# Optimization experiments

Measured on AMD Instinct MI355X. Metric: run time of the kernel, lower is better.

The kernel has to match this reference:

```python
import jax, jax.numpy as jnp
import numpy as np
import math

B, S, D, H = 2, 2048, 2048, 16
HD = D // H  # head_dim = 128


def _rope_tables(seq_len, head_dim, theta=10000.0):
    inv = 1.0 / (theta ** (np.arange(0, head_dim, 2, dtype=np.float32) / head_dim))
    t = np.arange(seq_len, dtype=np.float32)
    freqs = np.outer(t, inv)  # [S, HD/2]
    return jnp.asarray(np.cos(freqs)), jnp.asarray(np.sin(freqs))


def setup_inputs() -> dict:
    key = jax.random.key(0)
    ks = jax.random.split(key, 6)
    std = 1.0 / math.sqrt(D)
    x = jax.random.normal(ks[0], (B, S, D), dtype=jnp.float32)
    wq_w = jax.random.normal(ks[1], (D, D), dtype=jnp.float32) * std
    wk_w = jax.random.normal(ks[2], (D, D), dtype=jnp.float32) * std
    wv_w = jax.random.normal(ks[3], (D, D), dtype=jnp.float32) * std
    wo_w = jax.random.normal(ks[4], (D, D), dtype=jnp.float32) * std
    zb = jnp.zeros((D,), dtype=jnp.float32)
    fc, fs = _rope_tables(S, HD)
    return {"x": x, "wq_w": wq_w, "wq_b": zb, "wk_w": wk_w, "wk_b": zb,
            "wv_w": wv_w, "wv_b": zb, "wo_w": wo_w, "wo_b": zb,
            "freqs_cos": fc, "freqs_sin": fs}


def _apply_rope(q, k, cos, sin):
    # q, k: [B, S, H, HD]; cos/sin: [S, HD/2] -> broadcast [1, S, 1, HD/2]
    cos = cos[None, :, None, :]
    sin = sin[None, :, None, :]

    def rot(t):
        tr, ti = t[..., 0::2], t[..., 1::2]
        orr = tr * cos - ti * sin
        oi = tr * sin + ti * cos
        return jnp.stack([orr, oi], axis=-1).reshape(t.shape)

    return rot(q), rot(k)


def reference(x, wq_w, wq_b, wk_w, wk_b, wv_w, wv_b, wo_w, wo_b, freqs_cos, freqs_sin):
    b, s, d = x.shape
    q = (x @ wq_w.T + wq_b).reshape(b, s, H, HD)
    k = (x @ wk_w.T + wk_b).reshape(b, s, H, HD)
    v = (x @ wv_w.T + wv_b).reshape(b, s, H, HD)
    q, k = _apply_rope(q, k, freqs_cos[:s], freqs_sin[:s])
    q = q.transpose(0, 2, 1, 3)  # [B,H,S,HD]
    k = k.transpose(0, 2, 1, 3)
    v = v.transpose(0, 2, 1, 3)
    scale = math.sqrt(HD)
    scores = jnp.einsum('bhqd,bhkd->bhqk', q, k) / scale
    causal = jnp.tril(jnp.ones((s, s), dtype=bool))
    scores = jnp.where(causal[None, None], scores, jnp.float32(-jnp.inf))
    attn = jax.nn.softmax(scores, axis=-1)
    out = jnp.einsum('bhqk,bhkd->bhqd', attn, v)
    out = out.transpose(0, 2, 1, 3).reshape(b, s, d)
    out = out @ wo_w.T + wo_b
    return out, k, v
```

## Files before the change

### kernel.cpp

```cpp
#include <hip/hip_runtime.h>

#define B_  2
#define S_  2048
#define D_  2048
#define H_  16
#define HD_ 128

#define QSCALE 0.1275174319003887f

typedef __attribute__((ext_vector_type(4))) float  f32x4;
typedef __attribute__((ext_vector_type(8))) short  short8;
typedef __attribute__((ext_vector_type(8))) __bf16 bf16x8;
typedef __attribute__((ext_vector_type(4))) float  floatv4;
typedef __attribute__((ext_vector_type(4))) unsigned short ushortv4;

__device__ inline unsigned short f2bf(float f) {
  unsigned int u = __builtin_bit_cast(unsigned int, f);
  u += 0x7fffu + ((u >> 16) & 1u);
  return (unsigned short)(u >> 16);
}

__device__ inline void gld16(void* lds, const void* g) {
  __builtin_amdgcn_global_load_lds(
      (const __attribute__((address_space(1))) unsigned int*)g,
      (__attribute__((address_space(3))) unsigned int*)lds, 16, 0, 0);
}

__device__ inline bf16x8 lds_frag_b(const void* p) {
  return __builtin_bit_cast(bf16x8, *(const short8*)p);
}

__global__ void cvt_all(const float* __restrict__ x,
                        const float* __restrict__ w0, const float* __restrict__ w1,
                        const float* __restrict__ w2, const float* __restrict__ w3,
                        unsigned short* __restrict__ xb,
                        unsigned short* __restrict__ wb0, unsigned short* __restrict__ wb1,
                        unsigned short* __restrict__ wb2, unsigned short* __restrict__ wb3) {
  int i = blockIdx.x * 256 + threadIdx.x;
  const float* s; unsigned short* d; int off;
  if (i < 2097152) { s = x; d = xb; off = i; }
  else {
    int j = i - 2097152;
    int r = j >> 20; off = j & 1048575;
    s = (r == 0) ? w0 : (r == 1) ? w1 : (r == 2) ? w2 : w3;
    d = (r == 0) ? wb0 : (r == 1) ? wb1 : (r == 2) ? wb2 : wb3;
  }
  floatv4 v = ((const floatv4*)s)[off];
  ushortv4 o;
  o.x = f2bf(v.x); o.y = f2bf(v.y); o.z = f2bf(v.z); o.w = f2bf(v.w);
  ((ushortv4*)d)[off] = o;
}

template<int MI0, int NJ0>
__device__ inline void quad_mm(f32x4 (&acc)[4][4], const bf16x8 (&af)[2][2], const bf16x8 (&bf)[2][2]) {
#pragma unroll
  for (int mi = 0; mi < 2; ++mi)
#pragma unroll
    for (int nj = 0; nj < 2; ++nj)
#pragma unroll
      for (int ks = 0; ks < 2; ++ks)
        acc[MI0 + mi][NJ0 + nj] =
            __builtin_amdgcn_mfma_f32_16x16x32_bf16(af[mi][ks], bf[nj][ks], acc[MI0 + mi][NJ0 + nj], 0, 0, 0);
}

__device__ inline void stage(char* ldsbuf, int chunk, const char* gtile, int w, long thrOff) {
  gld16(ldsbuf + chunk * 8192 + w * 1024, gtile + (long)chunk * 64 * 4096 + thrOff);
}

#define RDF(dst, buf, baserow)                                                          \
  do {                                                                                  \
    int _r0 = (baserow);                                                                \
    _Pragma("unroll") for (int _ii = 0; _ii < 2; ++_ii) {                               \
      int _row = _r0 + _ii * 16;                                                        \
      _Pragma("unroll") for (int _ks = 0; _ks < 2; ++_ks)                               \
          dst[_ii][_ks] = lds_frag_b((buf) + _row * 128 + ((_ks * 64 + quad * 16) ^ xsw)); \
    }                                                                                   \
  } while (0)

#define GBAR() __builtin_amdgcn_s_barrier()
#define LGK0()                                                 \
  do {                                                         \
    asm volatile("s_waitcnt lgkmcnt(0)" ::: "memory");         \
    __builtin_amdgcn_sched_barrier(0);                         \
  } while (0)

template<int MODE>
__global__ __launch_bounds__(512, 1)
void gemm8p(const unsigned short* __restrict__ A,
            const unsigned short* __restrict__ W,
            const float* __restrict__ b0, const float* __restrict__ b1, const float* __restrict__ b2,
            float* __restrict__ CQ,
            float* __restrict__ CK,
            float* __restrict__ v_out,
            int nbx) {
  __shared__ __attribute__((aligned(16))) char smem[98304];
  char* As0 = smem;
  char* As1 = smem + 32768;
  char* Bs0 = smem + 65536;
  char* Bs1 = smem + 81920;

  const int t = threadIdx.x, w = t >> 6, lane = t & 63;
  const int quad = lane >> 4, l16 = lane & 15;
  const int wm = (w >> 1) * 64, wn = (w & 1) * 64;
  const int xsw = (l16 & 7) << 4;

  const int nwg = gridDim.x, q8 = nwg >> 3;
  const int wg = ((int)blockIdx.x & 7) * q8 + ((int)blockIdx.x >> 3);
  const int by = wg / nbx, bx = wg % nbx;
  const int m0 = by * 256, n0 = bx * 128;

  const char* Agl = (const char*)A + (size_t)m0 * 4096;
  const char* Wgl = (const char*)W + (size_t)n0 * 4096;
  const int sr = t >> 3;
  const long thrOff = (long)sr * 4096 + (((t & 7) * 16) ^ ((sr & 7) << 4));

#pragma unroll
  for (int c = 0; c < 4; ++c) stage(As0, c, Agl, w, thrOff);
#pragma unroll
  for (int c = 0; c < 2; ++c) stage(Bs0, c, Wgl, w, thrOff);
#pragma unroll
  for (int c = 0; c < 4; ++c) stage(As1, c, Agl + 128, w, thrOff);
  asm volatile("s_waitcnt vmcnt(4)" ::: "memory");
  GBAR();

  f32x4 acc[4][4] = {};

  for (int it = 0; it < 16; ++it) {
    int s0p = 2 * it + 2; if (s0p >= 32) s0p -= 2;
    int s1p = 2 * it + 3; if (s1p >= 32) s1p -= 2;
    const char* gB1  = Wgl + (long)(2 * it + 1) * 128;
    const char* gA0p = Agl + (long)s0p * 128;
    const char* gB0p = Wgl + (long)s0p * 128;
    const char* gA1p = Agl + (long)s1p * 128;
    bf16x8 a01[2][2], a23[2][2], b01[2][2], b23[2][2];

    stage(Bs1, 0, gB1, w, thrOff); stage(Bs1, 1, gB1, w, thrOff);
    RDF(a01, As0, wm + l16);
    RDF(a23, As0, wm + 32 + l16);
    RDF(b01, Bs0, wn + l16);
    GBAR(); LGK0();
    __builtin_amdgcn_s_setprio(1);
    quad_mm<0, 0>(acc, a01, b01); quad_mm<2, 0>(acc, a23, b01);
    __builtin_amdgcn_s_setprio(0);
    GBAR();
    RDF(b23, Bs0, wn + 32 + l16);
    stage(As0, 0, gA0p, w, thrOff); stage(As0, 1, gA0p, w, thrOff);
    stage(As0, 2, gA0p, w, thrOff); stage(As0, 3, gA0p, w, thrOff);
    GBAR(); LGK0();
    __builtin_amdgcn_s_setprio(1);
    quad_mm<0, 2>(acc, a01, b23); quad_mm<2, 2>(acc, a23, b23);
    __builtin_amdgcn_s_setprio(0);
    asm volatile("s_waitcnt vmcnt(4)" ::: "memory");
    GBAR();
    RDF(a01, As1, wm + l16);
    RDF(a23, As1, wm + 32 + l16);
    RDF(b01, Bs1, wn + l16);
    stage(Bs0, 0, gB0p, w, thrOff); stage(Bs0, 1, gB0p, w, thrOff);
    GBAR(); LGK0();
    __builtin_amdgcn_s_setprio(1);
    quad_mm<0, 0>(acc, a01, b01); quad_mm<2, 0>(acc, a23, b01);
    __builtin_amdgcn_s_setprio(0);
    GBAR();
    RDF(b23, Bs1, wn + 32 + l16);
    stage(As1, 0, gA1p, w, thrOff); stage(As1, 1, gA1p, w, thrOff);
    stage(As1, 2, gA1p, w, thrOff); stage(As1, 3, gA1p, w, thrOff);
    GBAR(); LGK0();
    __builtin_amdgcn_s_setprio(1);
    quad_mm<0, 2>(acc, a01, b23); quad_mm<2, 2>(acc, a23, b23);
    __builtin_amdgcn_s_setprio(0);
    asm volatile("s_waitcnt vmcnt(4)" ::: "memory");
    GBAR();
  }

  asm volatile("s_waitcnt vmcnt(0)" ::: "memory");

  if constexpr (MODE == 1) {
#pragma unroll
    for (int nj = 0; nj < 4; ++nj) {
      int col = n0 + wn + nj * 16 + l16;
      int sel = col >> 11;
      int cc  = col & 2047;
      const float* bp = (sel == 0) ? b0 : (sel == 1) ? b1 : b2;
      float bv = bp[cc];
#pragma unroll
      for (int mi = 0; mi < 4; ++mi)
#pragma unroll
        for (int r = 0; r < 4; ++r) {
          int row = m0 + wm + mi * 16 + quad * 4 + r;
          float v = acc[mi][nj][r] + bv;
          if (sel == 0) {
            CQ[(size_t)row * 2048 + cc] = v;
          } else if (sel == 1) {
            CK[(size_t)row * 2048 + cc] = v;
          } else {
            int s = row & 2047, bb = row >> 11;
            int hh = cc >> 7, d = cc & 127;
            v_out[((size_t)(bb * H_ + hh) * S_ + s) * HD_ + d] = v;
          }
        }
    }
  } else {
#pragma unroll
    for (int nj = 0; nj < 4; ++nj) {
      int col = n0 + wn + nj * 16 + l16;
      float bv = b0[col];
#pragma unroll
      for (int mi = 0; mi < 4; ++mi)
#pragma unroll
        for (int r = 0; r < 4; ++r) {
          int row = m0 + wm + mi * 16 + quad * 4 + r;
          CQ[(size_t)row * 2048 + col] = acc[mi][nj][r] + bv;
        }
    }
  }
}

__global__ void rope_kernel(const float* __restrict__ Qbuf,
                            const float* __restrict__ Kbuf,
                            const float* __restrict__ fc,
                            const float* __restrict__ fs,
                            unsigned short* __restrict__ Qa,
                            unsigned short* __restrict__ Ka,
                            float* __restrict__ k_out) {
  int idx = blockIdx.x * 256 + threadIdx.x;
  int i = idx & 63;
  int h = (idx >> 6) & (H_ - 1);
  int s = (idx >> 10) & (S_ - 1);
  int b = idx >> 21;
  size_t src = ((size_t)(b * S_ + s)) * D_ + h * HD_ + 2 * i;
  float2 q = *(const float2*)(Qbuf + src);
  float2 k = *(const float2*)(Kbuf + src);
  float c = fc[s * 64 + i], sn = fs[s * 64 + i];
  float qor = q.x * c - q.y * sn, qoi = q.x * sn + q.y * c;
  float kor = k.x * c - k.y * sn, koi = k.x * sn + k.y * c;
  size_t dst = ((size_t)((b * H_ + h) * S_ + s)) * HD_ + 2 * i;
  *(unsigned int*)(Qa + dst) = (unsigned int)f2bf(qor * QSCALE) | ((unsigned int)f2bf(qoi * QSCALE) << 16);
  *(unsigned int*)(Ka + dst) = (unsigned int)f2bf(kor) | ((unsigned int)f2bf(koi) << 16);
  *(float2*)(k_out + dst) = make_float2(kor, koi);
}

__global__ void vtrans_kernel(const float* __restrict__ Vsrc,
                              unsigned short* __restrict__ Vt) {
  __shared__ float tile[64][33];
  int t = threadIdx.x;
  int s0 = blockIdx.x * 64, d0 = blockIdx.y * 32, bh = blockIdx.z;
#pragma unroll
  for (int rr = 0; rr < 8; ++rr) {
    int sl = rr * 8 + (t >> 5), dl = t & 31;
    tile[sl][dl] = Vsrc[((size_t)(bh * S_ + s0 + sl)) * HD_ + d0 + dl];
  }
  __syncthreads();
#pragma unroll
  for (int rr = 0; rr < 8; ++rr) {
    int dl = rr * 4 + (t >> 6), sl = t & 63;
    Vt[((size_t)(bh * HD_ + d0 + dl)) * S_ + s0 + sl] = f2bf(tile[sl][dl]);
  }
}

__global__ __launch_bounds__(256, 2)
void attn_kernel(const unsigned short* __restrict__ Qa,
                 const unsigned short* __restrict__ Ka,
                 const unsigned short* __restrict__ Vt,
                 unsigned short* __restrict__ Oa) {
  __shared__ __attribute__((aligned(16))) unsigned short Ks[2][64 * 128];
  __shared__ __attribute__((aligned(16))) unsigned short Vs[128 * 64];
  __shared__ __attribute__((aligned(16))) unsigned short Ps[4][16 * 64];
  const int t = threadIdx.x, w = t >> 6, lane = t & 63;
  const int quad = lane >> 4, l16 = lane & 15;
  const int bid = blockIdx.x;
  const int bh = (bid & 7) + 8 * (bid >> 7);
  const int p  = (bid >> 3) & 15;
  const int b = bh >> 4, h = bh & 15;
  const unsigned short* Qp = Qa + (size_t)bh * S_ * HD_;
  const unsigned short* Kp = Ka + (size_t)bh * S_ * HD_;
  const unsigned short* Vp = Vt + (size_t)bh * HD_ * S_;
  const float NEGINF = -__builtin_inff();

  for (int part = 0; part < 2; ++part) {
    const int qs = part ? (31 - p) : p;
    const int q0 = qs * 64;
    const int ntmax = qs;

    __syncthreads();

#pragma unroll
    for (int j = 0; j < 4; ++j) {
      int o = (t + 256 * j) * 16;
      int row = o >> 8, cb = (o & 255) ^ ((row & 7) << 4);
      gld16((char*)Ks[0] + w * 1024 + j * 4096, (const char*)(Kp + (size_t)row * HD_) + cb);
    }
    bf16x8 qf[4];
#pragma unroll
    for (int kk = 0; kk < 4; ++kk)
      qf[kk] = *(const bf16x8*)(Qp + (size_t)(q0 + w * 16 + l16) * HD_ + kk * 32 + quad * 8);

    float m_i[4], l_i[4];
#pragma unroll
    for (int r = 0; r < 4; ++r) { m_i[r] = NEGINF; l_i[r] = 0.f; }
    f32x4 oacc[8] = {};
    int c = 0;

    for (int nt = 0; nt <= ntmax; ++nt) {
      __syncthreads();

#pragma unroll
      for (int j = 0; j < 4; ++j) {
        int o = (t + 256 * j) * 16;
        int vrow = o >> 7, vcb = (o & 127) ^ ((vrow & 7) << 4);
        gld16((char*)Vs + w * 1024 + j * 4096,
              (const char*)(Vp + (size_t)vrow * S_ + nt * 64) + vcb);
      }

      f32x4 sacc[4] = {};
      const char* Kc = (const char*)Ks[c];
#pragma unroll
      for (int j = 0; j < 4; ++j) {
        int krow = j * 16 + l16;
        const char* kbase = Kc + krow * 256;
        int ksw = (krow & 7) << 4;
#pragma unroll
        for (int kk = 0; kk < 4; ++kk) {
          bf16x8 kf = lds_frag_b(kbase + ((kk * 64 + quad * 16) ^ ksw));
          sacc[j] = __builtin_amdgcn_mfma_f32_16x16x32_bf16(qf[kk], kf, sacc[j], 0, 0, 0);
        }
      }

      const bool dotail = (nt == ntmax);
      float rowmax[4], alpha[4], rowsum[4];
#pragma unroll
      for (int r = 0; r < 4; ++r) rowmax[r] = NEGINF;
#pragma unroll
      for (int j = 0; j < 4; ++j) {
        int scol = nt * 64 + j * 16 + l16;
#pragma unroll
        for (int r = 0; r < 4; ++r) {
          float v = sacc[j][r];
          if (dotail && scol > q0 + w * 16 + quad * 4 + r) v = NEGINF;
          sacc[j][r] = v;
          rowmax[r] = fmaxf(rowmax[r], v);
        }
      }
#pragma unroll
      for (int off = 1; off < 16; off <<= 1)
#pragma unroll
        for (int r = 0; r < 4; ++r)
          rowmax[r] = fmaxf(rowmax[r], __shfl_xor(rowmax[r], off));
#pragma unroll
      for (int r = 0; r < 4; ++r) {
        float mnew = fmaxf(m_i[r], rowmax[r]);
        alpha[r] = __builtin_amdgcn_exp2f(m_i[r] - mnew);
        m_i[r] = mnew;
        rowsum[r] = 0.f;
      }
#pragma unroll
      for (int j = 0; j < 4; ++j)
#pragma unroll
        for (int r = 0; r < 4; ++r) {
          float e = __builtin_amdgcn_exp2f(sacc[j][r] - m_i[r]);
          sacc[j][r] = e;
          rowsum[r] += e;
        }
#pragma unroll
      for (int off = 1; off < 16; off <<= 1)
#pragma unroll
        for (int r = 0; r < 4; ++r)
          rowsum[r] += __shfl_xor(rowsum[r], off);
#pragma unroll
      for (int r = 0; r < 4; ++r) l_i[r] = l_i[r] * alpha[r] + rowsum[r];
#pragma unroll
      for (int f = 0; f < 8; ++f)
#pragma unroll
        for (int r = 0; r < 4; ++r) oacc[f][r] *= alpha[r];

      __syncthreads();

      if (nt < ntmax) {
#pragma unroll
        for (int j = 0; j < 4; ++j) {
          int o = (t + 256 * j) * 16;
          int row = o >> 8, cb = (o & 255) ^ ((row & 7) << 4);
          gld16((char*)Ks[c ^ 1] + w * 1024 + j * 4096,
                (const char*)(Kp + (size_t)((nt + 1) * 64 + row) * HD_) + cb);
        }
      }

      char* Pw = (char*)&Ps[w][0];
#pragma unroll
      for (int j = 0; j < 4; ++j)
#pragma unroll
        for (int r = 0; r < 4; ++r) {
          int prow = quad * 4 + r;
          *(unsigned short*)(Pw + prow * 128 + ((2 * (j * 16 + l16)) ^ ((prow & 7) << 4))) = f2bf(sacc[j][r]);
        }
      asm volatile("s_waitcnt lgkmcnt(0)" ::: "memory");

      const char* Vb = (const char*)Vs;
      int psw = (l16 & 7) << 4;
#pragma unroll
      for (int s2 = 0; s2 < 2; ++s2) {
        bf16x8 pf = lds_frag_b(Pw + l16 * 128 + ((s2 * 64 + quad * 16) ^ psw));
#pragma unroll
        for (int f = 0; f < 8; ++f) {
          int vrow = f * 16 + l16;
          bf16x8 vf = lds_frag_b(Vb + vrow * 128 + ((s2 * 64 + quad * 16) ^ ((vrow & 7) << 4)));
          oacc[f] = __builtin_amdgcn_mfma_f32_16x16x32_bf16(pf, vf, oacc[f], 0, 0, 0);
        }
      }
      c ^= 1;
    }

    float invl[4];
#pragma unroll
    for (int r = 0; r < 4; ++r) invl[r] = 1.f / l_i[r];
#pragma unroll
    for (int f = 0; f < 8; ++f)
#pragma unroll
      for (int r = 0; r < 4; ++r) {
        int srow = q0 + w * 16 + quad * 4 + r;
        int d = f * 16 + l16;
        Oa[((size_t)(b * S_ + srow)) * D_ + h * HD_ + d] = f2bf(oacc[f][r] * invl[r]);
      }
  }
}

extern "C" void kernel_launch(void* const* d_in, const int* in_sizes, int n_in,
                              void* d_out, int out_size, void* d_ws, size_t ws_size,
                              hipStream_t stream) {
  const float* x    = (const float*)d_in[0];
  const float* wq_w = (const float*)d_in[1];
  const float* wq_b = (const float*)d_in[2];
  const float* wk_w = (const float*)d_in[3];
  const float* wk_b = (const float*)d_in[4];
  const float* wv_w = (const float*)d_in[5];
  const float* wv_b = (const float*)d_in[6];
  const float* wo_w = (const float*)d_in[7];
  const float* wo_b = (const float*)d_in[8];
  const float* fc   = (const float*)d_in[9];
  const float* fs   = (const float*)d_in[10];

  float* out = (float*)d_out;
  const size_t BSD = (size_t)B_ * S_ * D_;
  float* k_out = out + BSD;
  float* v_out = out + 2 * BSD;

  char* ws = (char*)d_ws;
  unsigned short* xb   = (unsigned short*)(ws);
  unsigned short* wqb  = (unsigned short*)(ws + 16777216);
  unsigned short* wkb  = (unsigned short*)(ws + 25165824);
  unsigned short* wvb  = (unsigned short*)(ws + 33554432);
  unsigned short* wob  = (unsigned short*)(ws + 41943040);
  float*          Kbuf = (float*)(ws + 50331648);
  unsigned short* Qat  = (unsigned short*)(ws + 83886080);
  unsigned short* Kat  = (unsigned short*)(ws + 100663296);
  unsigned short* Vt   = (unsigned short*)(ws + 117440512);
  unsigned short* Ab   = (unsigned short*)(ws + 134217728);

  float* Qbuf = out;

  cvt_all<<<24576, 256, 0, stream>>>(x, wq_w, wk_w, wv_w, wo_w, xb, wqb, wkb, wvb, wob);

  gemm8p<1><<<dim3(768), 512, 0, stream>>>(xb, wqb, wq_b, wk_b, wv_b,
                                           Qbuf, Kbuf, v_out, 48);

  rope_kernel<<<16384, 256, 0, stream>>>(Qbuf, Kbuf, fc, fs, Qat, Kat, k_out);
  vtrans_kernel<<<dim3(32, 4, 32), 256, 0, stream>>>(v_out, Vt);
  attn_kernel<<<512, 256, 0, stream>>>(Qat, Kat, Vt, Ab);

  gemm8p<0><<<dim3(256), 512, 0, stream>>>(Ab, wob, wo_b, nullptr, nullptr,
                                           out, nullptr, nullptr, 16);
}
```

Before: 438.9 us.

## Interleave GEMM MFMA phases with finer staging and skip softmax rescale when max unchanged

The projection GEMM main loop is restructured so each quad_mm is a separate barrier-delimited phase, with LDS fragment reads and global-to-LDS staging spread across those phases. The B tile for the next step is also prefetched one stage earlier, so the vmcnt waits become 6. The aim is better overlap of memory traffic with MFMA work. In the attention kernel, the online-softmax rescale of l and oacc is skipped when no row maximum in the wave grows, which saves exp and multiply work on most tiles. The cost is a divergent branch and more barriers per GEMM iteration.

New measurement: 462.3 us. +5.3%, slower.

```diff
diff --git a/kernel.cpp b/kernel.cpp
--- a/kernel.cpp
+++ b/kernel.cpp
@@ -120,55 +120,61 @@
   for (int c = 0; c < 2; ++c) stage(Bs0, c, Wgl, w, thrOff);
 #pragma unroll
   for (int c = 0; c < 4; ++c) stage(As1, c, Agl + 128, w, thrOff);
-  asm volatile("s_waitcnt vmcnt(4)" ::: "memory");
+#pragma unroll
+  for (int c = 0; c < 2; ++c) stage(Bs1, c, Wgl + 128, w, thrOff);
+  asm volatile("s_waitcnt vmcnt(6)" ::: "memory");
   GBAR();
 
   f32x4 acc[4][4] = {};
 
   for (int it = 0; it < 16; ++it) {
-    int s0p = 2 * it + 2; if (s0p >= 32) s0p -= 2;
-    int s1p = 2 * it + 3; if (s1p >= 32) s1p -= 2;
-    const char* gB1  = Wgl + (long)(2 * it + 1) * 128;
-    const char* gA0p = Agl + (long)s0p * 128;
-    const char* gB0p = Wgl + (long)s0p * 128;
-    const char* gA1p = Agl + (long)s1p * 128;
+    int s0 = 2 * it + 2; if (s0 >= 32) s0 -= 2;
+    int s1 = 2 * it + 3; if (s1 >= 32) s1 -= 2;
+    const char* As0g = Agl + (long)s0 * 128;
+    const char* Bs0g = Wgl + (long)s0 * 128;
+    const char* As1g = Agl + (long)s1 * 128;
+    const char* Bs1g = Wgl + (long)s1 * 128;
     bf16x8 a01[2][2], a23[2][2], b01[2][2], b23[2][2];
 
-    stage(Bs1, 0, gB1, w, thrOff); stage(Bs1, 1, gB1, w, thrOff);
     RDF(a01, As0, wm + l16);
+    RDF(b01, Bs0, wn + l16);
+    GBAR(); LGK0();
+    __builtin_amdgcn_s_setprio(1); quad_mm<0, 0>(acc, a01, b01); __builtin_amdgcn_s_setprio(0);
+    GBAR();
     RDF(a23, As0, wm + 32 + l16);
-    RDF(b01, Bs0, wn + l16);
-    GBAR(); LGK0();
-    __builtin_amdgcn_s_setprio(1);
-    quad_mm<0, 0>(acc, a01, b01); quad_mm<2, 0>(acc, a23, b01);
-    __builtin_amdgcn_s_setprio(0);
+    GBAR(); LGK0();
+    __builtin_amdgcn_s_setprio(1); quad_mm<2, 0>(acc, a23, b01); __builtin_amdgcn_s_setprio(0);
     GBAR();
     RDF(b23, Bs0, wn + 32 + l16);
-    stage(As0, 0, gA0p, w, thrOff); stage(As0, 1, gA0p, w, thrOff);
-    stage(As0, 2, gA0p, w, thrOff); stage(As0, 3, gA0p, w, thrOff);
-    GBAR(); LGK0();
-    __builtin_amdgcn_s_setprio(1);
-    quad_mm<0, 2>(acc, a01, b23); quad_mm<2, 2>(acc, a23, b23);
-    __builtin_amdgcn_s_setprio(0);
+    stage(As0, 0, As0g, w, thrOff); stage(As0, 1, As0g, w, thrOff);
+    GBAR(); LGK0();
+    __builtin_amdgcn_s_setprio(1); quad_mm<0, 2>(acc, a01, b23); __builtin_amdgcn_s_setprio(0);
+    GBAR();
+    stage(As0, 2, As0g, w, thrOff); stage(As0, 3, As0g, w, thrOff);
+    GBAR(); LGK0();
+    __builtin_amdgcn_s_setprio(1); quad_mm<2, 2>(acc, a23, b23); __builtin_amdgcn_s_setprio(0);
     asm volatile("s_waitcnt vmcnt(4)" ::: "memory");
     GBAR();
     RDF(a01, As1, wm + l16);
+    RDF(b01, Bs1, wn + l16);
+    stage(Bs0, 0, Bs0g, w, thrOff); stage(Bs0, 1, Bs0g, w, thrOff);
+    GBAR(); LGK0();
+    __builtin_amdgcn_s_setprio(1); quad_mm<0, 0>(acc, a01, b01); __builtin_amdgcn_s_setprio(0);
+    GBAR();
     RDF(a23, As1, wm + 32 + l16);
-    RDF(b01, Bs1, wn + l16);
-    stage(Bs0, 0, gB0p, w, thrOff); stage(Bs0, 1, gB0p, w, thrOff);
-    GBAR(); LGK0();
-    __builtin_amdgcn_s_setprio(1);
-    quad_mm<0, 0>(acc, a01, b01); quad_mm<2, 0>(acc, a23, b01);
-    __builtin_amdgcn_s_setprio(0);
+    GBAR(); LGK0();
+    __builtin_amdgcn_s_setprio(1); quad_mm<2, 0>(acc, a23, b01); __builtin_amdgcn_s_setprio(0);
     GBAR();
     RDF(b23, Bs1, wn + 32 + l16);
-    stage(As1, 0, gA1p, w, thrOff); stage(As1, 1, gA1p, w, thrOff);
-    stage(As1, 2, gA1p, w, thrOff); stage(As1, 3, gA1p, w, thrOff);
-    GBAR(); LGK0();
-    __builtin_amdgcn_s_setprio(1);
-    quad_mm<0, 2>(acc, a01, b23); quad_mm<2, 2>(acc, a23, b23);
-    __builtin_amdgcn_s_setprio(0);
-    asm volatile("s_waitcnt vmcnt(4)" ::: "memory");
+    stage(As1, 0, As1g, w, thrOff); stage(As1, 1, As1g, w, thrOff);
+    GBAR(); LGK0();
+    __builtin_amdgcn_s_setprio(1); quad_mm<0, 2>(acc, a01, b23); __builtin_amdgcn_s_setprio(0);
+    GBAR();
+    stage(As1, 2, As1g, w, thrOff); stage(As1, 3, As1g, w, thrOff);
+    stage(Bs1, 0, Bs1g, w, thrOff); stage(Bs1, 1, Bs1g, w, thrOff);
+    GBAR(); LGK0();
+    __builtin_amdgcn_s_setprio(1); quad_mm<2, 2>(acc, a23, b23); __builtin_amdgcn_s_setprio(0);
+    asm volatile("s_waitcnt vmcnt(6)" ::: "memory");
     GBAR();
   }
 
@@ -326,7 +332,7 @@
       }
 
       const bool dotail = (nt == ntmax);
-      float rowmax[4], alpha[4], rowsum[4];
+      float rowmax[4], rowsum[4];
 #pragma unroll
       for (int r = 0; r < 4; ++r) rowmax[r] = NEGINF;
 #pragma unroll
@@ -345,13 +351,26 @@
 #pragma unroll
         for (int r = 0; r < 4; ++r)
           rowmax[r] = fmaxf(rowmax[r], __shfl_xor(rowmax[r], off));
-#pragma unroll
-      for (int r = 0; r < 4; ++r) {
-        float mnew = fmaxf(m_i[r], rowmax[r]);
-        alpha[r] = __builtin_amdgcn_exp2f(m_i[r] - mnew);
-        m_i[r] = mnew;
-        rowsum[r] = 0.f;
-      }
+
+      bool grow = false;
+#pragma unroll
+      for (int r = 0; r < 4; ++r) grow = grow || (rowmax[r] > m_i[r]);
+      if (__any(grow)) {
+        float alpha[4];
+#pragma unroll
+        for (int r = 0; r < 4; ++r) {
+          float mnew = fmaxf(m_i[r], rowmax[r]);
+          alpha[r] = __builtin_amdgcn_exp2f(m_i[r] - mnew);
+          m_i[r] = mnew;
+          l_i[r] *= alpha[r];
+        }
+#pragma unroll
+        for (int f = 0; f < 8; ++f)
+#pragma unroll
+          for (int r = 0; r < 4; ++r) oacc[f][r] *= alpha[r];
+      }
+#pragma unroll
+      for (int r = 0; r < 4; ++r) rowsum[r] = 0.f;
 #pragma unroll
       for (int j = 0; j < 4; ++j)
 #pragma unroll
@@ -366,11 +385,7 @@
         for (int r = 0; r < 4; ++r)
           rowsum[r] += __shfl_xor(rowsum[r], off);
 #pragma unroll
-      for (int r = 0; r < 4; ++r) l_i[r] = l_i[r] * alpha[r] + rowsum[r];
-#pragma unroll
-      for (int f = 0; f < 8; ++f)
-#pragma unroll
-        for (int r = 0; r < 4; ++r) oacc[f][r] *= alpha[r];
+      for (int r = 0; r < 4; ++r) l_i[r] += rowsum[r];
 
       __syncthreads();
 
```
